# Kernel tuning notes

Measured on AMD Instinct MI355X. Metric: run time of the kernel, lower is better.

The kernel has to match this reference:

```python
import jax, jax.numpy as jnp
import numpy as np

DIM = 512; HEADS = 8; DH = 64; M = 256; ITERS = 6; N_PATCH = 10000; N_CLASSES = 2


def layernorm(x, w, b, eps=1e-5):
    mu = x.mean(-1, keepdims=True)
    var = ((x - mu) ** 2).mean(-1, keepdims=True)
    return (x - mu) * jax.lax.rsqrt(var + eps) * w + b


def pinv_iter(x, iters=ITERS):
    # Moore-Penrose iterative pseudo-inverse (lucidrains nystrom-attention)
    abs_x = jnp.abs(x)
    col = abs_x.sum(-1)
    row = abs_x.sum(-2)
    z = jnp.swapaxes(x, -1, -2) / (jnp.max(col) * jnp.max(row))
    I = jnp.eye(x.shape[-1], dtype=x.dtype)
    for _ in range(iters):
        xz = x @ z
        z = 0.25 * z @ (13 * I - xz @ (15 * I - xz @ (7 * I - xz)))
    return z


def nystrom_attn(x, qkv_w, out_w, out_b, res_w):
    b, n, _ = x.shape
    pad = (-n) % M  # front-pad so n divisible by num_landmarks
    xp = jnp.pad(x, ((0, 0), (pad, 0), (0, 0)))
    npad = n + pad
    qkv = (xp @ qkv_w).reshape(b, npad, 3, HEADS, DH)
    q = jnp.transpose(qkv[:, :, 0], (0, 2, 1, 3)) * (DH ** -0.5)  # [b,h,n,d]
    k = jnp.transpose(qkv[:, :, 1], (0, 2, 1, 3))
    v = jnp.transpose(qkv[:, :, 2], (0, 2, 1, 3))
    l = npad // M
    q_l = q.reshape(b, HEADS, M, l, DH).mean(3)  # landmark means [b,h,m,d]
    k_l = k.reshape(b, HEADS, M, l, DH).mean(3)
    attn1 = jax.nn.softmax(jnp.einsum('bhnd,bhmd->bhnm', q, k_l), -1)
    attn2 = jax.nn.softmax(jnp.einsum('bhid,bhjd->bhij', q_l, k_l), -1)
    attn3 = jax.nn.softmax(jnp.einsum('bhmd,bhnd->bhmn', q_l, k), -1)
    out = (attn1 @ pinv_iter(attn2)) @ (attn3 @ v)  # [b,h,n,d]
    pk = (res_w.shape[2] - 1) // 2
    out = out + jax.lax.conv_general_dilated(
        v, res_w, (1, 1), [(pk, pk), (0, 0)], feature_group_count=HEADS)
    out = jnp.transpose(out, (0, 2, 1, 3)).reshape(b, npad, HEADS * DH)
    out = out @ out_w + out_b
    return out[:, -n:]


def ppeg(x, H, W, w7, b7, w5, b5, w3, b3):
    B, _, C = x.shape
    cls_tok, feat = x[:, :1], x[:, 1:]
    f = jnp.transpose(feat, (0, 2, 1)).reshape(B, C, H, W)
    def dw(w, b):
        p = w.shape[2] // 2
        return jax.lax.conv_general_dilated(
            f, w, (1, 1), [(p, p), (p, p)], feature_group_count=C) + b[None, :, None, None]
    y = f + dw(w7, b7) + dw(w5, b5) + dw(w3, b3)
    y = jnp.transpose(y.reshape(B, C, H * W), (0, 2, 1))
    return jnp.concatenate([cls_tok, y], axis=1)


def setup_inputs() -> dict:
    key = jax.random.key(0)
    ks = jax.random.split(key, 16)
    d = {
        'x': jax.random.normal(ks[0], (1, N_PATCH, DIM), jnp.float32),
        'cls_token': jax.random.normal(ks[1], (1, 1, DIM), jnp.float32) * 1e-6,
        'ln1_w': jnp.ones((DIM,), jnp.float32), 'ln1_b': jnp.zeros((DIM,), jnp.float32),
        'qkv1_w': jax.random.normal(ks[2], (DIM, 3 * DIM), jnp.float32) * 0.03,
        'out1_w': jax.random.normal(ks[3], (DIM, DIM), jnp.float32) * 0.04,
        'out1_b': jnp.zeros((DIM,), jnp.float32),
        'res1_w': jax.random.normal(ks[4], (HEADS, 1, 33, 1), jnp.float32) * 0.1,
        'p7_w': jax.random.normal(ks[5], (DIM, 1, 7, 7), jnp.float32) * 0.1,
        'p7_b': jnp.zeros((DIM,), jnp.float32),
        'p5_w': jax.random.normal(ks[6], (DIM, 1, 5, 5), jnp.float32) * 0.1,
        'p5_b': jnp.zeros((DIM,), jnp.float32),
        'p3_w': jax.random.normal(ks[7], (DIM, 1, 3, 3), jnp.float32) * 0.1,
        'p3_b': jnp.zeros((DIM,), jnp.float32),
        'ln2_w': jnp.ones((DIM,), jnp.float32), 'ln2_b': jnp.zeros((DIM,), jnp.float32),
        'qkv2_w': jax.random.normal(ks[8], (DIM, 3 * DIM), jnp.float32) * 0.03,
        'out2_w': jax.random.normal(ks[9], (DIM, DIM), jnp.float32) * 0.04,
        'out2_b': jnp.zeros((DIM,), jnp.float32),
        'res2_w': jax.random.normal(ks[10], (HEADS, 1, 33, 1), jnp.float32) * 0.1,
        'norm_w': jnp.ones((DIM,), jnp.float32), 'norm_b': jnp.zeros((DIM,), jnp.float32),
        'fc2_w': jax.random.normal(ks[11], (DIM, N_CLASSES), jnp.float32) * 0.06,
        'fc2_b': jnp.zeros((N_CLASSES,), jnp.float32),
        'pc_w': jax.random.normal(ks[12], (DIM, N_CLASSES), jnp.float32) * 0.06,
        'pc_b': jnp.zeros((N_CLASSES,), jnp.float32),
    }
    return d


def reference(x, cls_token, ln1_w, ln1_b, qkv1_w, out1_w, out1_b, res1_w,
              p7_w, p7_b, p5_w, p5_b, p3_w, p3_b,
              ln2_w, ln2_b, qkv2_w, out2_w, out2_b, res2_w,
              norm_w, norm_b, fc2_w, fc2_b, pc_w, pc_b):
    h = x.astype(jnp.float32)
    B, n0, C = h.shape
    _H = int(np.ceil(np.sqrt(n0))); _W = _H
    add = _H * _W - n0
    if add > 0:
        h = jnp.concatenate([h, h[:, :add]], axis=1)
    h = jnp.concatenate([jnp.broadcast_to(cls_token, (B, 1, C)), h], axis=1)
    h = h + nystrom_attn(layernorm(h, ln1_w, ln1_b), qkv1_w, out1_w, out1_b, res1_w)
    h = ppeg(h, _H, _W, p7_w, p7_b, p5_w, p5_b, p3_w, p3_b)
    h = h + nystrom_attn(layernorm(h, ln2_w, ln2_b), qkv2_w, out2_w, out2_b, res2_w)
    hn = layernorm(h, norm_w, norm_b)
    cls_f = hn[:, 0]
    patch_f = hn[:, 1:]
    if add > 0:
        patch_f = patch_f[:, :n0]
    bag_logits = cls_f @ fc2_w + fc2_b
    patch_logits = patch_f @ pc_w + pc_b
    patch_scores = jax.nn.softmax(patch_logits, -1)
    return bag_logits, patch_logits, patch_scores
```

## Files before the change

### kernel.cpp

```cpp
#include <hip/hip_runtime.h>
#include <hip/hip_bf16.h>

#define DIM    512
#define HEADS  8
#define DHD    64
#define MLAND  256
#define NTOK   10001
#define NPATCH 10000
#define NPAD   10240
#define PADR   239
#define LFAC   40
#define MOUT   10112
#define NSPLIT 8

typedef __bf16 bf16x8_t __attribute__((ext_vector_type(8)));
typedef float  f32x4_t  __attribute__((ext_vector_type(4)));
typedef short  short8_t __attribute__((ext_vector_type(8)));

__device__ inline bf16x8_t bzero8() {
    union { short8_t s; bf16x8_t b; } u;
    u.s = (short8_t){0, 0, 0, 0, 0, 0, 0, 0};
    return u.b;
}

#define GLDS(gp, lp) __builtin_amdgcn_global_load_lds( \
    (const __attribute__((address_space(1))) void*)(gp), \
    (__attribute__((address_space(3))) void*)(lp), 16, 0, 0)

__global__ void k_concat(const float* __restrict__ x, const float* __restrict__ cls,
                         float* __restrict__ h) {
    int idx = blockIdx.x * 256 + threadIdx.x;
    if (idx >= NTOK * DIM) return;
    int row = idx / DIM, col = idx % DIM;
    h[idx] = (row == 0) ? cls[col] : x[(row - 1) * DIM + col];
}

__global__ void k_layernorm_bf(const float* __restrict__ h, const float* __restrict__ w,
                               const float* __restrict__ b, __hip_bfloat16* __restrict__ xbf) {
    int row = blockIdx.x;
    const float* r = h + (long)row * DIM;
    int t = threadIdx.x;
    float v0 = r[t], v1 = r[t + 256];
    __shared__ float red[256];
    red[t] = v0 + v1; __syncthreads();
    for (int o = 128; o > 0; o >>= 1) { if (t < o) red[t] += red[t + o]; __syncthreads(); }
    float mu = red[0] * (1.f / DIM); __syncthreads();
    float d0 = v0 - mu, d1 = v1 - mu;
    red[t] = d0 * d0 + d1 * d1; __syncthreads();
    for (int o = 128; o > 0; o >>= 1) { if (t < o) red[t] += red[t + o]; __syncthreads(); }
    float rstd = rsqrtf(red[0] * (1.f / DIM) + 1e-5f);
    long base = (long)(PADR + row) * DIM;
    xbf[base + t]       = __float2bfloat16(d0 * rstd * w[t] + b[t]);
    xbf[base + t + 256] = __float2bfloat16(d1 * rstd * w[t + 256] + b[t + 256]);
}

__global__ void k_zerobf(__hip_bfloat16* __restrict__ p, int n) {
    int i = blockIdx.x * 256 + threadIdx.x;
    if (i < n) p[i] = __float2bfloat16(0.f);
}
__global__ void k_wt_cvt(const float* __restrict__ W, __hip_bfloat16* __restrict__ Wt,
                         int K, int N) {
    __shared__ float tile[32][33];
    int k0 = blockIdx.x * 32, n0 = blockIdx.y * 32;
    int lx = threadIdx.x % 32, ly = threadIdx.x / 32;
    for (int i = 0; i < 32; i += 8) tile[ly + i][lx] = W[(long)(k0 + ly + i) * N + n0 + lx];
    __syncthreads();
    for (int i = 0; i < 32; i += 8)
        Wt[(long)(n0 + ly + i) * K + k0 + lx] = __float2bfloat16(tile[lx][ly + i]);
}
__global__ void k_vt(const __hip_bfloat16* __restrict__ vh, __hip_bfloat16* __restrict__ vt) {
    __shared__ __hip_bfloat16 tile[32][33];
    int n0 = blockIdx.x * 32, d0 = blockIdx.y * 32, h = blockIdx.z;
    int lx = threadIdx.x % 32, ly = threadIdx.x / 32;
    for (int i = 0; i < 32; i += 8)
        tile[ly + i][lx] = vh[((long)h * NPAD + n0 + ly + i) * 64 + d0 + lx];
    __syncthreads();
    for (int i = 0; i < 32; i += 8)
        vt[((long)h * 64 + d0 + ly + i) * NPAD + n0 + lx] = tile[lx][ly + i];
}

__global__ __launch_bounds__(256) void k_qkv_gemm(
    const __hip_bfloat16* __restrict__ A, const __hip_bfloat16* __restrict__ Bt,
    __hip_bfloat16* __restrict__ qh, __hip_bfloat16* __restrict__ kh,
    __hip_bfloat16* __restrict__ vh)
{
    const int K = 512;
    __shared__ unsigned short As[128 * 64];
    __shared__ unsigned short Bs[128 * 64];
    int tid = threadIdx.x;
    int m0 = blockIdx.y * 128, n0 = blockIdx.x * 128;
    int wave = tid >> 6, lane = tid & 63;
    int wm = (wave & 1) * 64, wn = (wave >> 1) * 64;
    f32x4_t zero4 = {0.f, 0.f, 0.f, 0.f};
    f32x4_t acc[4][4];
#pragma unroll
    for (int i = 0; i < 4; i++)
#pragma unroll
        for (int j = 0; j < 4; j++) acc[i][j] = zero4;
    int quad = lane >> 4, fr = lane & 15;
    int lrow8 = lane >> 3, gls = lane & 7;
    int gg = gls ^ lrow8;

    for (int k0 = 0; k0 < K; k0 += 64) {
        __syncthreads();
#pragma unroll
        for (int rnd = 0; rnd < 4; rnd++) {
            int r0 = rnd * 32 + wave * 8;
            int ar = r0 + lrow8;
            GLDS(A  + (long)(m0 + ar) * K + k0 + gg * 8, &As[r0 * 64]);
            GLDS(Bt + (long)(n0 + ar) * K + k0 + gg * 8, &Bs[r0 * 64]);
        }
        __syncthreads();
#pragma unroll
        for (int ks = 0; ks < 2; ks++) {
            int sg = (ks * 4 + quad) ^ (fr & 7);
            bf16x8_t af[4], bq[4];
#pragma unroll
            for (int i = 0; i < 4; i++) {
                af[i] = *(const bf16x8_t*)&As[(wm + i * 16 + fr) * 64 + sg * 8];
                bq[i] = *(const bf16x8_t*)&Bs[(wn + i * 16 + fr) * 64 + sg * 8];
            }
#pragma unroll
            for (int i = 0; i < 4; i++)
#pragma unroll
                for (int j = 0; j < 4; j++)
                    acc[i][j] = __builtin_amdgcn_mfma_f32_16x16x32_bf16(af[i], bq[j], acc[i][j], 0, 0, 0);
        }
    }
    int col = lane & 15, rq = lane >> 4;
#pragma unroll
    for (int j = 0; j < 4; j++) {
        int c = n0 + wn + j * 16 + col;
        int sect = c >> 9;
        int hh = (c >> 6) & 7;
        int d = c & 63;
        __hip_bfloat16* dst = (sect == 0) ? qh : (sect == 1) ? kh : vh;
        float sc = (sect == 0) ? 0.125f : 1.f;
#pragma unroll
        for (int i = 0; i < 4; i++) {
            int rbase = m0 + wm + i * 16 + rq * 4;
#pragma unroll
            for (int rr = 0; rr < 4; rr++) {
                int r = rbase + rr;
                dst[((long)hh * NPAD + r) * 64 + d] = __float2bfloat16(acc[i][j][rr] * sc);
            }
        }
    }
}

__global__ __launch_bounds__(256) void k_mfma_gemm(
    const __hip_bfloat16* __restrict__ A, const __hip_bfloat16* __restrict__ Bt,
    float* __restrict__ C, int M, int N, int K, int Mstore,
    const float* __restrict__ bias, int accum)
{
    __shared__ unsigned short As[128 * 64];
    __shared__ unsigned short Bs[128 * 64];
    int tid = threadIdx.x;
    int m0 = blockIdx.y * 128, n0 = blockIdx.x * 128;
    int wave = tid >> 6, lane = tid & 63;
    int wm = (wave & 1) * 64, wn = (wave >> 1) * 64;
    f32x4_t zero4 = {0.f, 0.f, 0.f, 0.f};
    f32x4_t acc[4][4];
#pragma unroll
    for (int i = 0; i < 4; i++)
#pragma unroll
        for (int j = 0; j < 4; j++) acc[i][j] = zero4;
    int quad = lane >> 4, fr = lane & 15;
    int lrow8 = lane >> 3, gls = lane & 7;
    int gg = gls ^ lrow8;

    for (int k0 = 0; k0 < K; k0 += 64) {
        __syncthreads();
#pragma unroll
        for (int rnd = 0; rnd < 4; rnd++) {
            int r0 = rnd * 32 + wave * 8;
            int ar = r0 + lrow8;
            GLDS(A  + (long)(m0 + ar) * K + k0 + gg * 8, &As[r0 * 64]);
            GLDS(Bt + (long)(n0 + ar) * K + k0 + gg * 8, &Bs[r0 * 64]);
        }
        __syncthreads();
#pragma unroll
        for (int ks = 0; ks < 2; ks++) {
            int sg = (ks * 4 + quad) ^ (fr & 7);
            bf16x8_t af[4], bq[4];
#pragma unroll
            for (int i = 0; i < 4; i++) {
                af[i] = *(const bf16x8_t*)&As[(wm + i * 16 + fr) * 64 + sg * 8];
                bq[i] = *(const bf16x8_t*)&Bs[(wn + i * 16 + fr) * 64 + sg * 8];
            }
#pragma unroll
            for (int i = 0; i < 4; i++)
#pragma unroll
                for (int j = 0; j < 4; j++)
                    acc[i][j] = __builtin_amdgcn_mfma_f32_16x16x32_bf16(af[i], bq[j], acc[i][j], 0, 0, 0);
        }
    }
    int col = lane & 15, rq = lane >> 4;
#pragma unroll
    for (int j = 0; j < 4; j++) {
        int c = n0 + wn + j * 16 + col;
        float bsv = bias ? bias[c] : 0.f;
#pragma unroll
        for (int i = 0; i < 4; i++) {
            int rbase = m0 + wm + i * 16 + rq * 4;
#pragma unroll
            for (int rr = 0; rr < 4; rr++) {
                int r = rbase + rr;
                if (r >= Mstore) continue;
                float v = acc[i][j][rr] + bsv;
                long off = (long)r * N + c;
                if (accum) C[off] += v; else C[off] = v;
            }
        }
    }
}

__global__ __launch_bounds__(256) void k_mfma_t64(
    const __hip_bfloat16* __restrict__ A, long lda, long abatch, int arowmax,
    const __hip_bfloat16* __restrict__ Bt, long ldb, long bbatch,
    __hip_bfloat16* __restrict__ Cbf, long ldc, long cbatch, int ksplit)
{
    int h = blockIdx.z;
    const __hip_bfloat16* Ab = A + (long)h * abatch;
    const __hip_bfloat16* Bb = Bt + (long)h * bbatch;
    int m0 = blockIdx.y * 128;
    int kbeg = blockIdx.x * ksplit, kend = kbeg + ksplit;
    int wave = threadIdx.x >> 6, lane = threadIdx.x & 63;
    int wm = (wave & 1) * 64, wn = (wave >> 1) * 32;
    int fr = lane & 15, quad = lane >> 4;
    f32x4_t zero4 = {0.f, 0.f, 0.f, 0.f};
    f32x4_t acc[4][2];
#pragma unroll
    for (int i = 0; i < 4; i++) { acc[i][0] = zero4; acc[i][1] = zero4; }
    for (int k0 = kbeg; k0 < kend; k0 += 32) {
        bf16x8_t bq[2];
#pragma unroll
        for (int j = 0; j < 2; j++)
            bq[j] = *(const bf16x8_t*)(Bb + (long)(wn + j * 16 + fr) * ldb + k0 + quad * 8);
#pragma unroll
        for (int i = 0; i < 4; i++) {
            int r = m0 + wm + i * 16 + fr;
            bf16x8_t af = (r < arowmax) ? *(const bf16x8_t*)(Ab + (long)r * lda + k0 + quad * 8)
                                        : bzero8();
#pragma unroll
            for (int j = 0; j < 2; j++)
                acc[i][j] = __builtin_amdgcn_mfma_f32_16x16x32_bf16(af, bq[j], acc[i][j], 0, 0, 0);
        }
    }
#pragma unroll
    for (int i = 0; i < 4; i++)
#pragma unroll
        for (int j = 0; j < 2; j++)
#pragma unroll
            for (int rr = 0; rr < 4; rr++) {
                int r = m0 + wm + i * 16 + quad * 4 + rr;
                int c = wn + j * 16 + fr;
                Cbf[(long)h * cbatch + (long)c * ldc + r] = __float2bfloat16(acc[i][j][rr]);
            }
}

__global__ __launch_bounds__(256) void k_mm256(
    const __hip_bfloat16* __restrict__ Aa, const __hip_bfloat16* __restrict__ Bt,
    float s, float acoef, const __hip_bfloat16* __restrict__ Aadd,
    __hip_bfloat16* __restrict__ Ca, __hip_bfloat16* __restrict__ Ct)
{
    int hd = blockIdx.z;
    long hb = (long)hd * 65536;
    int m0 = blockIdx.y * 64, n0 = blockIdx.x * 32;
    int wave = threadIdx.x >> 6, lane = threadIdx.x & 63;
    int fr = lane & 15, quad = lane >> 4;
    int mrow = m0 + wave * 16;
    f32x4_t zero4 = {0.f, 0.f, 0.f, 0.f};
    f32x4_t acc[2];
    acc[0] = zero4; acc[1] = zero4;
#pragma unroll
    for (int k0 = 0; k0 < 256; k0 += 32) {
        bf16x8_t af = *(const bf16x8_t*)(Aa + hb + (long)(mrow + fr) * 256 + k0 + quad * 8);
#pragma unroll
        for (int j = 0; j < 2; j++) {
            bf16x8_t bq = *(const bf16x8_t*)(Bt + hb + (long)(n0 + j * 16 + fr) * 256 + k0 + quad * 8);
            acc[j] = __builtin_amdgcn_mfma_f32_16x16x32_bf16(af, bq, acc[j], 0, 0, 0);
        }
    }
#pragma unroll
    for (int j = 0; j < 2; j++)
#pragma unroll
        for (int rr = 0; rr < 4; rr++) {
            int r = mrow + quad * 4 + rr;
            int c = n0 + j * 16 + fr;
            float v = s * acc[j][rr];
            if (Aadd) v += acoef * __bfloat162float(Aadd[hb + (long)r * 256 + c]);
            __hip_bfloat16 bv = __float2bfloat16(v);
            if (Ca) Ca[hb + (long)r * 256 + c] = bv;
            if (Ct) Ct[hb + (long)c * 256 + r] = bv;
        }
}

__global__ __launch_bounds__(256) void k_attn3f(
    const __hip_bfloat16* __restrict__ qlbf, const __hip_bfloat16* __restrict__ kh,
    const __hip_bfloat16* __restrict__ vt, float* __restrict__ part)
{
    int ns = blockIdx.x, mt = blockIdx.y, h = blockIdx.z;
    int wave = threadIdx.x >> 6, lane = threadIdx.x & 63;
    int fr = lane & 15, quad = lane >> 4;
    int lrow8 = lane >> 3, gls = lane & 7;
    int gg = gls ^ lrow8;
    int vsub = lane >> 5, vgrp = lane & 31;
    int swz = fr & 7;
    __shared__ unsigned short Ks[2][256 * 64];
    __shared__ unsigned short Vs[2][64 * 256];
    __shared__ __hip_bfloat16 Pl[64 * 136];
    f32x4_t zero4 = {0.f, 0.f, 0.f, 0.f};
    bf16x8_t aq[2];
    {
        const __hip_bfloat16* qb = qlbf + (long)h * 16384 + (long)(mt * 64 + wave * 16 + fr) * 64;
        aq[0] = *(const bf16x8_t*)(qb + quad * 8);
        aq[1] = *(const bf16x8_t*)(qb + 32 + quad * 8);
    }
    f32x4_t O[4];
#pragma unroll
    for (int j = 0; j < 4; j++) O[j] = zero4;
    float mr[4] = {-1e30f, -1e30f, -1e30f, -1e30f};
    float lr[4] = {0.f, 0.f, 0.f, 0.f};
    const __hip_bfloat16* kb = kh + (long)h * NPAD * 64;
    const __hip_bfloat16* vb = vt + (long)h * 64 * NPAD;

#define STAGE_KV(N0, KD, VD) do { \
    _Pragma("unroll") \
    for (int rnd = 0; rnd < 8; rnd++) { \
        int r0 = rnd * 32 + wave * 8; \
        GLDS(kb + (long)((N0) + r0 + lrow8) * 64 + gg * 8, (KD) + r0 * 64); \
    } \
    _Pragma("unroll") \
    for (int rnd = 0; rnd < 8; rnd++) { \
        int v0 = rnd * 8 + wave * 2; \
        int vrow = v0 + vsub; \
        GLDS(vb + (long)vrow * NPAD + (N0) + (vgrp ^ (vrow & 7)) * 8, (VD) + v0 * 256); \
    } \
} while (0)

    STAGE_KV(ns * 1280, &Ks[0][0], &Vs[0][0]);

    for (int nt = 0; nt < 5; nt++) {
        int bsel = nt & 1;
        if (nt < 4) {
            int n1 = ns * 1280 + (nt + 1) * 256;
            STAGE_KV(n1, &Ks[bsel ^ 1][0], &Vs[bsel ^ 1][0]);
            asm volatile("s_waitcnt vmcnt(16)" ::: "memory");
        } else {
            asm volatile("s_waitcnt vmcnt(0)" ::: "memory");
        }
        __builtin_amdgcn_s_barrier();

        const unsigned short* Kc = &Ks[bsel][0];
        const unsigned short* Vc = &Vs[bsel][0];
        f32x4_t s[16];
#pragma unroll
        for (int j = 0; j < 16; j++) s[j] = zero4;
#pragma unroll
        for (int j = 0; j < 16; j++) {
            const unsigned short* kr = Kc + (j * 16 + fr) * 64;
            bf16x8_t b0 = *(const bf16x8_t*)(kr + (quad ^ swz) * 8);
            bf16x8_t b1 = *(const bf16x8_t*)(kr + ((quad ^ swz) ^ 4) * 8);
            s[j] = __builtin_amdgcn_mfma_f32_16x16x32_bf16(aq[0], b0, s[j], 0, 0, 0);
            s[j] = __builtin_amdgcn_mfma_f32_16x16x32_bf16(aq[1], b1, s[j], 0, 0, 0);
        }
        float tm[4] = {-1e30f, -1e30f, -1e30f, -1e30f};
#pragma unroll
        for (int j = 0; j < 16; j++)
#pragma unroll
            for (int rr = 0; rr < 4; rr++) tm[rr] = fmaxf(tm[rr], s[j][rr]);
#pragma unroll
        for (int rr = 0; rr < 4; rr++) {
#pragma unroll
            for (int o = 8; o > 0; o >>= 1) tm[rr] = fmaxf(tm[rr], __shfl_xor(tm[rr], o));
        }
        float alpha[4], ts[4];
#pragma unroll
        for (int rr = 0; rr < 4; rr++) {
            float mnew = fmaxf(mr[rr], tm[rr]);
            alpha[rr] = __expf(mr[rr] - mnew);
            mr[rr] = mnew;
            ts[rr] = 0.f;
        }
#pragma unroll
        for (int j = 0; j < 16; j++)
#pragma unroll
            for (int rr = 0; rr < 4; rr++) {
                float e = __expf(s[j][rr] - mr[rr]);
                s[j][rr] = e;
                ts[rr] += e;
            }
#pragma unroll
        for (int rr = 0; rr < 4; rr++) {
#pragma unroll
            for (int o = 8; o > 0; o >>= 1) ts[rr] += __shfl_xor(ts[rr], o);
            lr[rr] = lr[rr] * alpha[rr] + ts[rr];
        }
#pragma unroll
        for (int j = 0; j < 4; j++)
#pragma unroll
            for (int rr = 0; rr < 4; rr++) O[j][rr] *= alpha[rr];
#pragma unroll
        for (int half = 0; half < 2; half++) {
#pragma unroll
            for (int j = 0; j < 8; j++)
#pragma unroll
                for (int rr = 0; rr < 4; rr++)
                    Pl[(wave * 16 + quad * 4 + rr) * 136 + j * 16 + fr] =
                        __float2bfloat16(s[half * 8 + j][rr]);
#pragma unroll
            for (int k0 = 0; k0 < 128; k0 += 32) {
                bf16x8_t af = *(const bf16x8_t*)&Pl[(wave * 16 + fr) * 136 + k0 + quad * 8];
                int gb = (half * 128 + k0) >> 3;
#pragma unroll
                for (int j = 0; j < 4; j++) {
                    const unsigned short* vr = Vc + (j * 16 + fr) * 256;
                    bf16x8_t bq = *(const bf16x8_t*)(vr + ((gb + quad) ^ swz) * 8);
                    O[j] = __builtin_amdgcn_mfma_f32_16x16x32_bf16(af, bq, O[j], 0, 0, 0);
                }
            }
        }
        asm volatile("" ::: "memory");
        __builtin_amdgcn_s_barrier();
    }
#undef STAGE_KV

    float* Ob = part + (long)((h * 4 + mt) * NSPLIT + ns) * 4224;
#pragma unroll
    for (int j = 0; j < 4; j++)
#pragma unroll
        for (int rr = 0; rr < 4; rr++)
            Ob[(wave * 16 + quad * 4 + rr) * 64 + j * 16 + fr] = O[j][rr];
    if (fr == 0) {
#pragma unroll
        for (int rr = 0; rr < 4; rr++) {
            Ob[4096 + wave * 16 + quad * 4 + rr] = mr[rr];
            Ob[4160 + wave * 16 + quad * 4 + rr] = lr[rr];
        }
    }
}

__global__ void k_a3comb(const float* __restrict__ part, __hip_bfloat16* __restrict__ a3vt) {
    int mt = blockIdx.x, h = blockIdx.y, t = threadIdx.x;
    int row = t >> 2, c0 = (t & 3) * 16;
    long base = (long)((h * 4 + mt) * NSPLIT) * 4224;
    float M = -1e30f;
    for (int s = 0; s < NSPLIT; s++) M = fmaxf(M, part[base + s * 4224 + 4096 + row]);
    float L = 0.f;
    float o[16];
#pragma unroll
    for (int c = 0; c < 16; c++) o[c] = 0.f;
    for (int s = 0; s < NSPLIT; s++) {
        const float* pb = part + base + (long)s * 4224;
        float w = __expf(pb[4096 + row] - M);
        L += pb[4160 + row] * w;
#pragma unroll
        for (int c = 0; c < 16; c++) o[c] += w * pb[row * 64 + c0 + c];
    }
    float invL = 1.f / L;
#pragma unroll
    for (int c = 0; c < 16; c++)
        a3vt[(long)h * 16384 + (long)(c0 + c) * 256 + mt * 64 + row] = __float2bfloat16(o[c] * invL);
}

__global__ void k_conv_res(const __hip_bfloat16* __restrict__ vh, const float* __restrict__ resw,
                           __hip_bfloat16* __restrict__ convbf) {
    int e4 = blockIdx.x * 256 + threadIdx.x;
    if (e4 >= NTOK * 128) return;
    int i = e4 >> 7;
    int c4 = (e4 & 127) * 4;
    int hh = c4 >> 6, d = c4 & 63;
    int n = PADR + i;
    const __hip_bfloat16* vb = vh + (long)hh * NPAD * 64 + d;
    float a0 = 0.f, a1 = 0.f, a2 = 0.f, a3 = 0.f;
#pragma unroll
    for (int t = 0; t < 33; t++) {
        int nn = n - 16 + t;
        if (nn < NPAD) {
            float w = resw[hh * 33 + t];
            uint2 pv = *(const uint2*)(vb + (long)nn * 64);
            __hip_bfloat16 vv[4];
            *(uint2*)vv = pv;
            a0 += w * __bfloat162float(vv[0]);
            a1 += w * __bfloat162float(vv[1]);
            a2 += w * __bfloat162float(vv[2]);
            a3 += w * __bfloat162float(vv[3]);
        }
    }
    __hip_bfloat16 o[4] = {__float2bfloat16(a0), __float2bfloat16(a1),
                           __float2bfloat16(a2), __float2bfloat16(a3)};
    *(uint2*)(convbf + (long)i * DIM + c4) = *(uint2*)o;
}

__global__ __launch_bounds__(256, 4) void k_attn1f(
    const __hip_bfloat16* __restrict__ qh, const __hip_bfloat16* __restrict__ klbf,
    const __hip_bfloat16* __restrict__ w2bt, const __hip_bfloat16* __restrict__ convbf,
    __hip_bfloat16* __restrict__ abf)
{
    int h = blockIdx.y;
    int i0 = blockIdx.x * 32;
    __shared__ __hip_bfloat16 Pl[64 * 136];
    __shared__ float mS[2][2][16][2];
    int tid = threadIdx.x;
    int wave = tid >> 6, lane = tid & 63;
    int rg = wave & 1, lh = wave >> 1;
    int fr = lane & 15, quad = lane >> 4;
    const __hip_bfloat16* kb = klbf + (long)h * (MLAND * DHD) + (long)lh * 128 * DHD;
    f32x4_t zero4 = {0.f, 0.f, 0.f, 0.f};

    f32x4_t s[8];
#pragma unroll
    for (int j = 0; j < 8; j++) s[j] = zero4;
    int arow = i0 + rg * 16 + fr;
    const __hip_bfloat16* qrow = qh + ((long)h * NPAD + PADR + arow) * 64;
#pragma unroll
    for (int k0 = 0; k0 < 64; k0 += 32) {
        bf16x8_t af = (arow < NTOK) ? *(const bf16x8_t*)(qrow + k0 + quad * 8) : bzero8();
#pragma unroll
        for (int j = 0; j < 8; j++) {
            bf16x8_t bq = *(const bf16x8_t*)(kb + (long)(j * 16 + fr) * DHD + k0 + quad * 8);
            s[j] = __builtin_amdgcn_mfma_f32_16x16x32_bf16(af, bq, s[j], 0, 0, 0);
        }
    }
    float mx[4] = {-1e30f, -1e30f, -1e30f, -1e30f};
#pragma unroll
    for (int j = 0; j < 8; j++)
#pragma unroll
        for (int rr = 0; rr < 4; rr++) mx[rr] = fmaxf(mx[rr], s[j][rr]);
#pragma unroll
    for (int rr = 0; rr < 4; rr++) {
#pragma unroll
        for (int o = 8; o > 0; o >>= 1) mx[rr] = fmaxf(mx[rr], __shfl_xor(mx[rr], o));
    }
    float sum[4] = {0.f, 0.f, 0.f, 0.f};
#pragma unroll
    for (int j = 0; j < 8; j++)
#pragma unroll
        for (int rr = 0; rr < 4; rr++) {
            float e = __expf(s[j][rr] - mx[rr]);
            s[j][rr] = e;
            sum[rr] += e;
        }
#pragma unroll
    for (int rr = 0; rr < 4; rr++) {
#pragma unroll
        for (int o = 8; o > 0; o >>= 1) sum[rr] += __shfl_xor(sum[rr], o);
    }
    if (fr == 0) {
#pragma unroll
        for (int rr = 0; rr < 4; rr++) {
            mS[lh][rg][quad * 4 + rr][0] = mx[rr];
            mS[lh][rg][quad * 4 + rr][1] = sum[rr];
        }
    }
#pragma unroll
    for (int j = 0; j < 8; j++)
#pragma unroll
        for (int rr = 0; rr < 4; rr++)
            Pl[(wave * 16 + quad * 4 + rr) * 136 + j * 16 + fr] = __float2bfloat16(s[j][rr]);
    __syncthreads();
    float fac[4];
#pragma unroll
    for (int rr = 0; rr < 4; rr++) {
        int r16 = quad * 4 + rr;
        float pm = mS[lh ^ 1][rg][r16][0], pS = mS[lh ^ 1][rg][r16][1];
        float M = fmaxf(mx[rr], pm);
        float sw = __expf(mx[rr] - M);
        float tot = sum[rr] * sw + pS * __expf(pm - M);
        fac[rr] = sw / tot;
    }
    const __hip_bfloat16* wb = w2bt + (long)h * (DHD * MLAND) + lh * 128;
    f32x4_t oc[4];
#pragma unroll
    for (int j = 0; j < 4; j++) oc[j] = zero4;
#pragma unroll
    for (int k0 = 0; k0 < 128; k0 += 32) {
        bf16x8_t af = *(const bf16x8_t*)&Pl[(wave * 16 + fr) * 136 + k0 + quad * 8];
#pragma unroll
        for (int j = 0; j < 4; j++) {
            bf16x8_t bq = *(const bf16x8_t*)(wb + (long)(j * 16 + fr) * MLAND + k0 + quad * 8);
            oc[j] = __builtin_amdgcn_mfma_f32_16x16x32_bf16(af, bq, oc[j], 0, 0, 0);
        }
    }
#pragma unroll
    for (int j = 0; j < 4; j++)
#pragma unroll
        for (int rr = 0; rr < 4; rr++) oc[j][rr] *= fac[rr];
    __syncthreads();
    float* ex = (float*)Pl;
    if (lh == 1) {
#pragma unroll
        for (int j = 0; j < 4; j++)
#pragma unroll
            for (int rr = 0; rr < 4; rr++)
                ex[(rg * 16 + quad * 4 + rr) * 64 + j * 16 + fr] = oc[j][rr];
    }
    __syncthreads();
    if (lh == 0) {
        float cp[4][4];
#pragma unroll
        for (int j = 0; j < 4; j++)
#pragma unroll
            for (int rr = 0; rr < 4; rr++) {
                int r = i0 + rg * 16 + quad * 4 + rr;
                cp[j][rr] = (r < NTOK)
                    ? __bfloat162float(convbf[(long)r * DIM + h * DHD + j * 16 + fr]) : 0.f;
            }
#pragma unroll
        for (int j = 0; j < 4; j++)
#pragma unroll
            for (int rr = 0; rr < 4; rr++) {
                int r = i0 + rg * 16 + quad * 4 + rr;
                if (r < NTOK) {
                    float v = oc[j][rr] + ex[(rg * 16 + quad * 4 + rr) * 64 + j * 16 + fr]
                              + cp[j][rr];
                    abf[(long)r * DIM + h * DHD + j * 16 + fr] = __float2bfloat16(v);
                }
            }
    }
}

__global__ void k_landmarks(const __hip_bfloat16* __restrict__ qh,
                            const __hip_bfloat16* __restrict__ kh,
                            float* __restrict__ ql, float* __restrict__ kl,
                            __hip_bfloat16* __restrict__ qlbf, __hip_bfloat16* __restrict__ klbf) {
    int m = blockIdx.x, h = blockIdx.y, d = threadIdx.x;
    float sq = 0.f, sk = 0.f;
    for (int j = 0; j < LFAC; j++) {
        long base = ((long)h * NPAD + m * LFAC + j) * 64 + d;
        sq += __bfloat162float(qh[base]);
        sk += __bfloat162float(kh[base]);
    }
    long o = ((long)h * MLAND + m) * DHD + d;
    float vq = sq * (1.f / LFAC), vk = sk * (1.f / LFAC);
    ql[o] = vq; kl[o] = vk;
    qlbf[o] = __float2bfloat16(vq);
    klbf[o] = __float2bfloat16(vk);
}

__global__ void k_attn2(const float* __restrict__ ql, const float* __restrict__ kl,
                        float* __restrict__ attn2, __hip_bfloat16* __restrict__ attn2bf) {
    int i = blockIdx.x, h = blockIdx.y, j = threadIdx.x;
    __shared__ float q[64];
    __shared__ float red[256];
    if (j < 64) q[j] = ql[((long)h * MLAND + i) * DHD + j];
    __syncthreads();
    const float* kr = kl + ((long)h * MLAND + j) * DHD;
    float s = 0.f;
#pragma unroll 8
    for (int d = 0; d < 64; d++) s += q[d] * kr[d];
    red[j] = s; __syncthreads();
    for (int o = 128; o > 0; o >>= 1) { if (j < o) red[j] = fmaxf(red[j], red[j + o]); __syncthreads(); }
    float mx = red[0]; __syncthreads();
    float e = __expf(s - mx);
    red[j] = e; __syncthreads();
    for (int o = 128; o > 0; o >>= 1) { if (j < o) red[j] += red[j + o]; __syncthreads(); }
    float v = e / red[0];
    long off = ((long)h * MLAND + i) * MLAND + j;
    attn2[off] = v;
    attn2bf[off] = __float2bfloat16(v);
}

__global__ void k_colrow(const float* __restrict__ x, float* __restrict__ scal) {
    int h = blockIdx.x, t = threadIdx.x;
    const float* xh = x + (long)h * MLAND * MLAND;
    float cs = 0.f, rs = 0.f;
    for (int j = 0; j < MLAND; j++) {
        cs += fabsf(xh[(long)t * MLAND + j]);
        rs += fabsf(xh[(long)j * MLAND + t]);
    }
    __shared__ float red[256];
    red[t] = cs; __syncthreads();
    for (int o = 128; o > 0; o >>= 1) { if (t < o) red[t] = fmaxf(red[t], red[t + o]); __syncthreads(); }
    if (t == 0) scal[2 + h] = red[0];
    __syncthreads();
    red[t] = rs; __syncthreads();
    for (int o = 128; o > 0; o >>= 1) { if (t < o) red[t] = fmaxf(red[t], red[t + o]); __syncthreads(); }
    if (t == 0) scal[10 + h] = red[0];
}

__global__ void k_tscale2(const float* __restrict__ x, const float* __restrict__ scal,
                          __hip_bfloat16* __restrict__ za, __hip_bfloat16* __restrict__ zt) {
    int h = blockIdx.z;
    int tj = blockIdx.x * 32, ti = blockIdx.y * 32;
    __shared__ float tile[32][33];
    const float* xh = x + (long)h * 65536;
    int lx = threadIdx.x % 32, ly = threadIdx.x / 32;
    float cm = scal[2], rm = scal[10];
#pragma unroll
    for (int k = 1; k < 8; k++) {
        cm = fmaxf(cm, scal[2 + k]);
        rm = fmaxf(rm, scal[10 + k]);
    }
    float inv = 1.f / (cm * rm);
    for (int yy = 0; yy < 32; yy += 8) {
        float v = xh[(long)(ti + ly + yy) * MLAND + tj + lx];
        tile[ly + yy][lx] = v;
        zt[(long)h * 65536 + (long)(ti + ly + yy) * MLAND + tj + lx] = __float2bfloat16(v * inv);
    }
    __syncthreads();
    for (int yy = 0; yy < 32; yy += 8)
        za[(long)h * 65536 + (long)(tj + ly + yy) * MLAND + ti + lx] =
            __float2bfloat16(tile[lx][ly + yy] * inv);
}

__global__ void k_tfwd(const float* __restrict__ h, float* __restrict__ ft) {
    __shared__ float tile[32][33];
    int t0 = blockIdx.x * 32, c0 = blockIdx.y * 32;
    int lx = threadIdx.x % 32, ly = threadIdx.x / 32;
    for (int i = 0; i < 32; i += 8) {
        int t = t0 + ly + i;
        if (t < NPATCH) tile[ly + i][lx] = h[(long)(1 + t) * DIM + c0 + lx];
    }
    __syncthreads();
    for (int i = 0; i < 32; i += 8) {
        int c = c0 + ly + i, t = t0 + lx;
        if (t < NPATCH) ft[(long)c * NPATCH + t] = tile[lx][ly + i];
    }
}

__global__ __launch_bounds__(256) void k_ppeg2(
    const float* __restrict__ ft, float* __restrict__ yt,
    const float* __restrict__ w7, const float* __restrict__ b7,
    const float* __restrict__ w5, const float* __restrict__ b5,
    const float* __restrict__ w3, const float* __restrict__ b3)
{
    int s = blockIdx.x, c = blockIdx.y;
    __shared__ float tile[26][106];
    __shared__ float wt[49];
    int tid = threadIdx.x;
    int r0 = s * 20 - 3;
    for (int idx = tid; idx < 26 * 106; idx += 256) {
        int rr = idx / 106, cc = idx % 106;
        int gy = r0 + rr, gx = cc - 3;
        float v = 0.f;
        if (gy >= 0 && gy < 100 && gx >= 0 && gx < 100)
            v = ft[(long)c * NPATCH + gy * 100 + gx];
        tile[rr][cc] = v;
    }
    if (tid < 49) {
        int dy = tid / 7 - 3, dx = tid % 7 - 3;
        float w = w7[c * 49 + tid];
        if (dy >= -2 && dy <= 2 && dx >= -2 && dx <= 2) w += w5[c * 25 + (dy + 2) * 5 + (dx + 2)];
        if (dy >= -1 && dy <= 1 && dx >= -1 && dx <= 1) w += w3[c * 9 + (dy + 1) * 3 + (dx + 1)];
        wt[tid] = w;
    }
    __syncthreads();
    float bsum = b7[c] + b5[c] + b3[c];
    for (int p = tid; p < 2000; p += 256) {
        int ly = p / 100, lx = p % 100;
        float acc = tile[ly + 3][lx + 3] + bsum;
#pragma unroll
        for (int dy = 0; dy < 7; dy++)
#pragma unroll
            for (int dx = 0; dx < 7; dx++)
                acc += wt[dy * 7 + dx] * tile[ly + dy][lx + dx];
        yt[(long)c * NPATCH + (s * 20 + ly) * 100 + lx] = acc;
    }
}

__global__ void k_tback(const float* __restrict__ yt, float* __restrict__ h) {
    __shared__ float tile[32][33];
    int t0 = blockIdx.x * 32, c0 = blockIdx.y * 32;
    int lx = threadIdx.x % 32, ly = threadIdx.x / 32;
    for (int i = 0; i < 32; i += 8) {
        int c = c0 + ly + i, t = t0 + lx;
        if (t < NPATCH) tile[ly + i][lx] = yt[(long)c * NPATCH + t];
    }
    __syncthreads();
    for (int i = 0; i < 32; i += 8) {
        int t = t0 + ly + i;
        if (t < NPATCH) h[(long)(1 + t) * DIM + c0 + lx] = tile[lx][ly + i];
    }
}

__global__ void k_final(const float* __restrict__ h, const float* __restrict__ nw,
                        const float* __restrict__ nb,
                        const float* __restrict__ fc2w, const float* __restrict__ fc2b,
                        const float* __restrict__ pcw, const float* __restrict__ pcb,
                        float* __restrict__ out)
{
    int row = blockIdx.x;
    int t = threadIdx.x;
    const float* r = h + (long)row * DIM;
    float v0 = r[t], v1 = r[t + 256];
    __shared__ float red[256];
    red[t] = v0 + v1; __syncthreads();
    for (int o = 128; o > 0; o >>= 1) { if (t < o) red[t] += red[t + o]; __syncthreads(); }
    float mu = red[0] * (1.f / DIM); __syncthreads();
    float d0 = v0 - mu, d1 = v1 - mu;
    red[t] = d0 * d0 + d1 * d1; __syncthreads();
    for (int o = 128; o > 0; o >>= 1) { if (t < o) red[t] += red[t + o]; __syncthreads(); }
    float rstd = rsqrtf(red[0] * (1.f / DIM) + 1e-5f); __syncthreads();
    float h0 = d0 * rstd * nw[t] + nb[t];
    float h1 = d1 * rstd * nw[t + 256] + nb[t + 256];
    const float* w = (row == 0) ? fc2w : pcw;
    float p0 = h0 * w[t * 2] + h1 * w[(t + 256) * 2];
    float p1 = h0 * w[t * 2 + 1] + h1 * w[(t + 256) * 2 + 1];
    red[t] = p0; __syncthreads();
    for (int o = 128; o > 0; o >>= 1) { if (t < o) red[t] += red[t + o]; __syncthreads(); }
    float l0 = red[0]; __syncthreads();
    red[t] = p1; __syncthreads();
    for (int o = 128; o > 0; o >>= 1) { if (t < o) red[t] += red[t + o]; __syncthreads(); }
    if (t == 0) {
        float l1 = red[0];
        const float* bb = (row == 0) ? fc2b : pcb;
        float a0 = l0 + bb[0], a1 = l1 + bb[1];
        if (row == 0) { out[0] = a0; out[1] = a1; }
        else {
            long i = row - 1;
            out[2 + i * 2] = a0;
            out[2 + i * 2 + 1] = a1;
            float m = fmaxf(a0, a1);
            float e0 = __expf(a0 - m), e1 = __expf(a1 - m);
            float inv = 1.f / (e0 + e1);
            out[2 + 2 * NPATCH + i * 2] = e0 * inv;
            out[2 + 2 * NPATCH + i * 2 + 1] = e1 * inv;
        }
    }
}

extern "C" void kernel_launch(void* const* d_in, const int* in_sizes, int n_in,
                              void* d_out, int out_size, void* d_ws, size_t ws_size,
                              hipStream_t stream)
{
    const float* x     = (const float*)d_in[0];
    const float* cls   = (const float*)d_in[1];
    const float* ln1w  = (const float*)d_in[2];
    const float* ln1b  = (const float*)d_in[3];
    const float* qkv1w = (const float*)d_in[4];
    const float* out1w = (const float*)d_in[5];
    const float* out1b = (const float*)d_in[6];
    const float* res1w = (const float*)d_in[7];
    const float* p7w   = (const float*)d_in[8];
    const float* p7b   = (const float*)d_in[9];
    const float* p5w   = (const float*)d_in[10];
    const float* p5b   = (const float*)d_in[11];
    const float* p3w   = (const float*)d_in[12];
    const float* p3b   = (const float*)d_in[13];
    const float* ln2w  = (const float*)d_in[14];
    const float* ln2b  = (const float*)d_in[15];
    const float* qkv2w = (const float*)d_in[16];
    const float* out2w = (const float*)d_in[17];
    const float* out2b = (const float*)d_in[18];
    const float* res2w = (const float*)d_in[19];
    const float* normw = (const float*)d_in[20];
    const float* normb = (const float*)d_in[21];
    const float* fc2w  = (const float*)d_in[22];
    const float* fc2b  = (const float*)d_in[23];
    const float* pcw   = (const float*)d_in[24];
    const float* pcb   = (const float*)d_in[25];
    float* out = (float*)d_out;

    float* p = (float*)d_ws;
    float* h      = p; p += 5120512;
    float* yt     = p; p += 5120512;
    float* ql     = p; p += 131072;
    float* kl     = p; p += 131072;
    float* x2     = p; p += 524288;
    float* scal   = p; p += 32;
    float* part   = p; p += 1081344;
    float* ft     = p; p += 5120512;
    __hip_bfloat16* qh     = (__hip_bfloat16*)p; p += 2621440;
    __hip_bfloat16* kh     = (__hip_bfloat16*)p; p += 2621440;
    __hip_bfloat16* vh     = (__hip_bfloat16*)p; p += 2621440;
    __hip_bfloat16* xbf    = (__hip_bfloat16*)p; p += 2621440;
    __hip_bfloat16* abf    = (__hip_bfloat16*)p; p += 2588672;
    __hip_bfloat16* convbf = (__hip_bfloat16*)p; p += 2560256;
    __hip_bfloat16* qw1t   = (__hip_bfloat16*)p; p += 393216;
    __hip_bfloat16* qw2t   = (__hip_bfloat16*)p; p += 393216;
    __hip_bfloat16* ow1t   = (__hip_bfloat16*)p; p += 131072;
    __hip_bfloat16* ow2t   = (__hip_bfloat16*)p; p += 131072;
    __hip_bfloat16* x2a    = (__hip_bfloat16*)p; p += 262144;
    __hip_bfloat16* za     = (__hip_bfloat16*)p; p += 262144;
    __hip_bfloat16* zt     = (__hip_bfloat16*)p; p += 262144;
    __hip_bfloat16* za2    = (__hip_bfloat16*)p; p += 262144;
    __hip_bfloat16* zt2    = (__hip_bfloat16*)p; p += 262144;
    __hip_bfloat16* xza    = (__hip_bfloat16*)p; p += 262144;
    __hip_bfloat16* xzt    = (__hip_bfloat16*)p; p += 262144;
    __hip_bfloat16* t1t    = (__hip_bfloat16*)p; p += 262144;
    __hip_bfloat16* t2t    = (__hip_bfloat16*)p; p += 262144;
    __hip_bfloat16* qlbf   = (__hip_bfloat16*)p; p += 65536;
    __hip_bfloat16* klbf   = (__hip_bfloat16*)p; p += 65536;
    __hip_bfloat16* vt     = (__hip_bfloat16*)p; p += 2621440;
    __hip_bfloat16* a3vt   = (__hip_bfloat16*)p; p += 65536;
    __hip_bfloat16* w2bt   = (__hip_bfloat16*)p; p += 65536;

    k_concat<<<dim3((NTOK * DIM + 255) / 256), 256, 0, stream>>>(x, cls, h);
    k_wt_cvt<<<dim3(16, 48), 256, 0, stream>>>(qkv1w, qw1t, 512, 1536);
    k_wt_cvt<<<dim3(16, 48), 256, 0, stream>>>(qkv2w, qw2t, 512, 1536);
    k_wt_cvt<<<dim3(16, 16), 256, 0, stream>>>(out1w, ow1t, 512, 512);
    k_wt_cvt<<<dim3(16, 16), 256, 0, stream>>>(out2w, ow2t, 512, 512);
    k_zerobf<<<dim3((PADR * DIM + 255) / 256), 256, 0, stream>>>(xbf, PADR * DIM);

    auto layer = [&](const float* lnw, const float* lnb, const __hip_bfloat16* qwt,
                     const __hip_bfloat16* owt, const float* outb, const float* resw) {
        k_layernorm_bf<<<NTOK, 256, 0, stream>>>(h, lnw, lnb, xbf);
        k_qkv_gemm<<<dim3(12, 80), 256, 0, stream>>>(xbf, qwt, qh, kh, vh);
        k_vt<<<dim3(320, 2, HEADS), 256, 0, stream>>>(vh, vt);
        k_landmarks<<<dim3(MLAND, HEADS), 64, 0, stream>>>(qh, kh, ql, kl, qlbf, klbf);
        k_attn2<<<dim3(MLAND, HEADS), 256, 0, stream>>>(ql, kl, x2, x2a);
        k_colrow<<<HEADS, 256, 0, stream>>>(x2, scal);
        k_tscale2<<<dim3(8, 8, HEADS), 256, 0, stream>>>(x2, scal, za, zt);
        {
            __hip_bfloat16 *zra = za, *zrt = zt, *zoa = za2, *zot = zt2;
            dim3 g(8, 4, HEADS);
            for (int it = 0; it < 6; it++) {
                k_mm256<<<g, 256, 0, stream>>>(x2a, zrt, 1.f, 0.f, nullptr, xza, xzt);
                k_mm256<<<g, 256, 0, stream>>>(xza, xzt, -1.f, 7.f, xza, nullptr, t1t);
                k_mm256<<<g, 256, 0, stream>>>(xza, t1t, -1.f, 15.f, xza, nullptr, t2t);
                k_mm256<<<g, 256, 0, stream>>>(zra, t2t, -0.25f, 3.25f, zra, zoa, zot);
                __hip_bfloat16* tmp;
                tmp = zra; zra = zoa; zoa = tmp;
                tmp = zrt; zrt = zot; zot = tmp;
            }
        }
        k_attn3f<<<dim3(NSPLIT, 4, HEADS), 256, 0, stream>>>(qlbf, kh, vt, part);
        k_a3comb<<<dim3(4, HEADS), 256, 0, stream>>>(part, a3vt);
        k_mfma_t64<<<dim3(1, 2, HEADS), 256, 0, stream>>>(
            za, 256, 65536, 256, a3vt, 256, 16384,
            w2bt, 256, 16384, 256);
        k_conv_res<<<dim3((NTOK * 128 + 255) / 256), 256, 0, stream>>>(vh, resw, convbf);
        k_attn1f<<<dim3(313, HEADS), 256, 0, stream>>>(qh, klbf, w2bt, convbf, abf);
        k_mfma_gemm<<<dim3(4, 79), 256, 0, stream>>>(abf, owt, h, MOUT, 512, 512,
                                                     NTOK, outb, 1);
    };

    layer(ln1w, ln1b, qw1t, ow1t, out1b, res1w);

    k_tfwd<<<dim3(313, 16), 256, 0, stream>>>(h, ft);
    k_ppeg2<<<dim3(5, 512), 256, 0, stream>>>(ft, yt, p7w, p7b, p5w, p5b, p3w, p3b);
    k_tback<<<dim3(313, 16), 256, 0, stream>>>(yt, h);

    layer(ln2w, ln2b, qw2t, ow2t, out2b, res2w);

    k_final<<<NTOK, 256, 0, stream>>>(h, normw, normb, fc2w, fc2b, pcw, pcb, out);
    (void)in_sizes; (void)n_in; (void)out_size; (void)ws_size;
}
```

Baseline: 974.6 us.

## Fuse pseudo-inverse iterations into one persistent kernel with grid barriers

Replaces the 24 per-layer small GEMM launches of the Moore-Penrose iteration with a single persistent kernel. Its 256 blocks synchronise between phases through an atomic counter barrier, and the counter is reset inside k_tscale2. This removes launch and drain overhead between tiny dependent GEMMs, but it depends on every block being co-resident, since otherwise the barrier can deadlock. Separately, attn1f drops the max subtraction in its softmax and hoists the residual conv loads to the start of the kernel. Dropping the max saves shuffles and exps but risks fp32 overflow if logits ever get large.

```diff
diff --git a/kernel.cpp b/kernel.cpp
--- a/kernel.cpp
+++ b/kernel.cpp
@@ -259,17 +259,12 @@
             }
 }
 
-__global__ __launch_bounds__(256) void k_mm256(
-    const __hip_bfloat16* __restrict__ Aa, const __hip_bfloat16* __restrict__ Bt,
-    float s, float acoef, const __hip_bfloat16* __restrict__ Aadd,
-    __hip_bfloat16* __restrict__ Ca, __hip_bfloat16* __restrict__ Ct)
+__device__ __forceinline__ void mm_phase(
+    const __hip_bfloat16* Aa, const __hip_bfloat16* Bt,
+    float s, float acoef, const __hip_bfloat16* Aadd,
+    __hip_bfloat16* Ca, __hip_bfloat16* Ct,
+    long hb, int mrow, int n0, int fr, int quad)
 {
-    int hd = blockIdx.z;
-    long hb = (long)hd * 65536;
-    int m0 = blockIdx.y * 64, n0 = blockIdx.x * 32;
-    int wave = threadIdx.x >> 6, lane = threadIdx.x & 63;
-    int fr = lane & 15, quad = lane >> 4;
-    int mrow = m0 + wave * 16;
     f32x4_t zero4 = {0.f, 0.f, 0.f, 0.f};
     f32x4_t acc[2];
     acc[0] = zero4; acc[1] = zero4;
@@ -294,6 +289,49 @@
             if (Ca) Ca[hb + (long)r * 256 + c] = bv;
             if (Ct) Ct[hb + (long)c * 256 + r] = bv;
         }
+}
+
+__device__ __forceinline__ void pinv_sync(int* cnt, int target) {
+    __syncthreads();
+    __threadfence();
+    if (threadIdx.x == 0) {
+        __hip_atomic_fetch_add(cnt, 1, __ATOMIC_RELAXED, __HIP_MEMORY_SCOPE_AGENT);
+        while (__hip_atomic_load(cnt, __ATOMIC_RELAXED, __HIP_MEMORY_SCOPE_AGENT) < target)
+            __builtin_amdgcn_s_sleep(2);
+    }
+    __syncthreads();
+    __threadfence();
+}
+
+__global__ __launch_bounds__(256) void k_pinv(
+    const __hip_bfloat16* __restrict__ x2a,
+    __hip_bfloat16* __restrict__ za,  __hip_bfloat16* __restrict__ zt,
+    __hip_bfloat16* __restrict__ za2, __hip_bfloat16* __restrict__ zt2,
+    __hip_bfloat16* __restrict__ xza, __hip_bfloat16* __restrict__ xzt,
+    __hip_bfloat16* __restrict__ t1t, __hip_bfloat16* __restrict__ t2t,
+    int* cnt)
+{
+    int hd = blockIdx.z;
+    long hb = (long)hd * 65536;
+    int m0 = blockIdx.y * 64, n0 = blockIdx.x * 32;
+    int wave = threadIdx.x >> 6, lane = threadIdx.x & 63;
+    int fr = lane & 15, quad = lane >> 4;
+    int mrow = m0 + wave * 16;
+    __hip_bfloat16 *zra = za, *zrt = zt, *zoa = za2, *zot = zt2;
+    int ph = 0;
+    for (int it = 0; it < 6; it++) {
+        mm_phase(x2a, zrt, 1.f, 0.f, nullptr, xza, xzt, hb, mrow, n0, fr, quad);
+        pinv_sync(cnt, ++ph * 256);
+        mm_phase(xza, xzt, -1.f, 7.f, xza, nullptr, t1t, hb, mrow, n0, fr, quad);
+        pinv_sync(cnt, ++ph * 256);
+        mm_phase(xza, t1t, -1.f, 15.f, xza, nullptr, t2t, hb, mrow, n0, fr, quad);
+        pinv_sync(cnt, ++ph * 256);
+        mm_phase(zra, t2t, -0.25f, 3.25f, zra, zoa, zot, hb, mrow, n0, fr, quad);
+        if (it < 5) pinv_sync(cnt, ++ph * 256);
+        __hip_bfloat16* tmp;
+        tmp = zra; zra = zoa; zoa = tmp;
+        tmp = zrt; zrt = zot; zot = tmp;
+    }
 }
 
 __global__ __launch_bounds__(256) void k_attn3f(
@@ -501,7 +539,7 @@
     int h = blockIdx.y;
     int i0 = blockIdx.x * 32;
     __shared__ __hip_bfloat16 Pl[64 * 136];
-    __shared__ float mS[2][2][16][2];
+    __shared__ float mS[2][2][16];
     int tid = threadIdx.x;
     int wave = tid >> 6, lane = tid & 63;
     int rg = wave & 1, lh = wave >> 1;
@@ -509,96 +547,8 @@
     const __hip_bfloat16* kb = klbf + (long)h * (MLAND * DHD) + (long)lh * 128 * DHD;
     f32x4_t zero4 = {0.f, 0.f, 0.f, 0.f};
 
-    f32x4_t s[8];
-#pragma unroll
-    for (int j = 0; j < 8; j++) s[j] = zero4;
-    int arow = i0 + rg * 16 + fr;
-    const __hip_bfloat16* qrow = qh + ((long)h * NPAD + PADR + arow) * 64;
-#pragma unroll
-    for (int k0 = 0; k0 < 64; k0 += 32) {
-        bf16x8_t af = (arow < NTOK) ? *(const bf16x8_t*)(qrow + k0 + quad * 8) : bzero8();
-#pragma unroll
-        for (int j = 0; j < 8; j++) {
-            bf16x8_t bq = *(const bf16x8_t*)(kb + (long)(j * 16 + fr) * DHD + k0 + quad * 8);
-            s[j] = __builtin_amdgcn_mfma_f32_16x16x32_bf16(af, bq, s[j], 0, 0, 0);
-        }
-    }
-    float mx[4] = {-1e30f, -1e30f, -1e30f, -1e30f};
-#pragma unroll
-    for (int j = 0; j < 8; j++)
-#pragma unroll
-        for (int rr = 0; rr < 4; rr++) mx[rr] = fmaxf(mx[rr], s[j][rr]);
-#pragma unroll
-    for (int rr = 0; rr < 4; rr++) {
-#pragma unroll
-        for (int o = 8; o > 0; o >>= 1) mx[rr] = fmaxf(mx[rr], __shfl_xor(mx[rr], o));
-    }
-    float sum[4] = {0.f, 0.f, 0.f, 0.f};
-#pragma unroll
-    for (int j = 0; j < 8; j++)
-#pragma unroll
-        for (int rr = 0; rr < 4; rr++) {
-            float e = __expf(s[j][rr] - mx[rr]);
-            s[j][rr] = e;
-            sum[rr] += e;
-        }
-#pragma unroll
-    for (int rr = 0; rr < 4; rr++) {
-#pragma unroll
-        for (int o = 8; o > 0; o >>= 1) sum[rr] += __shfl_xor(sum[rr], o);
-    }
-    if (fr == 0) {
-#pragma unroll
-        for (int rr = 0; rr < 4; rr++) {
-            mS[lh][rg][quad * 4 + rr][0] = mx[rr];
-            mS[lh][rg][quad * 4 + rr][1] = sum[rr];
-        }
-    }
-#pragma unroll
-    for (int j = 0; j < 8; j++)
-#pragma unroll
-        for (int rr = 0; rr < 4; rr++)
-            Pl[(wave * 16 + quad * 4 + rr) * 136 + j * 16 + fr] = __float2bfloat16(s[j][rr]);
-    __syncthreads();
-    float fac[4];
-#pragma unroll
-    for (int rr = 0; rr < 4; rr++) {
-        int r16 = quad * 4 + rr;
-        float pm = mS[lh ^ 1][rg][r16][0], pS = mS[lh ^ 1][rg][r16][1];
-        float M = fmaxf(mx[rr], pm);
-        float sw = __expf(mx[rr] - M);
-        float tot = sum[rr] * sw + pS * __expf(pm - M);
-        fac[rr] = sw / tot;
-    }
-    const __hip_bfloat16* wb = w2bt + (long)h * (DHD * MLAND) + lh * 128;
-    f32x4_t oc[4];
-#pragma unroll
-    for (int j = 0; j < 4; j++) oc[j] = zero4;
-#pragma unroll
-    for (int k0 = 0; k0 < 128; k0 += 32) {
-        bf16x8_t af = *(const bf16x8_t*)&Pl[(wave * 16 + fr) * 136 + k0 + quad * 8];
-#pragma unroll
-        for (int j = 0; j < 4; j++) {
-            bf16x8_t bq = *(const bf16x8_t*)(wb + (long)(j * 16 + fr) * MLAND + k0 + quad * 8);
-            oc[j] = __builtin_amdgcn_mfma_f32_16x16x32_bf16(af, bq, oc[j], 0, 0, 0);
-        }
-    }
-#pragma unroll
-    for (int j = 0; j < 4; j++)
-#pragma unroll
-        for (int rr = 0; rr < 4; rr++) oc[j][rr] *= fac[rr];
-    __syncthreads();
-    float* ex = (float*)Pl;
-    if (lh == 1) {
-#pragma unroll
-        for (int j = 0; j < 4; j++)
-#pragma unroll
-            for (int rr = 0; rr < 4; rr++)
-                ex[(rg * 16 + quad * 4 + rr) * 64 + j * 16 + fr] = oc[j][rr];
-    }
-    __syncthreads();
+    float cp[4][4];
     if (lh == 0) {
-        float cp[4][4];
 #pragma unroll
         for (int j = 0; j < 4; j++)
 #pragma unroll
@@ -607,6 +557,78 @@
                 cp[j][rr] = (r < NTOK)
                     ? __bfloat162float(convbf[(long)r * DIM + h * DHD + j * 16 + fr]) : 0.f;
             }
+    }
+
+    f32x4_t s[8];
+#pragma unroll
+    for (int j = 0; j < 8; j++) s[j] = zero4;
+    int arow = i0 + rg * 16 + fr;
+    const __hip_bfloat16* qrow = qh + ((long)h * NPAD + PADR + arow) * 64;
+#pragma unroll
+    for (int k0 = 0; k0 < 64; k0 += 32) {
+        bf16x8_t af = (arow < NTOK) ? *(const bf16x8_t*)(qrow + k0 + quad * 8) : bzero8();
+#pragma unroll
+        for (int j = 0; j < 8; j++) {
+            bf16x8_t bq = *(const bf16x8_t*)(kb + (long)(j * 16 + fr) * DHD + k0 + quad * 8);
+            s[j] = __builtin_amdgcn_mfma_f32_16x16x32_bf16(af, bq, s[j], 0, 0, 0);
+        }
+    }
+    float sum[4] = {0.f, 0.f, 0.f, 0.f};
+#pragma unroll
+    for (int j = 0; j < 8; j++)
+#pragma unroll
+        for (int rr = 0; rr < 4; rr++) {
+            float e = __expf(s[j][rr]);
+            s[j][rr] = e;
+            sum[rr] += e;
+        }
+#pragma unroll
+    for (int rr = 0; rr < 4; rr++) {
+#pragma unroll
+        for (int o = 8; o > 0; o >>= 1) sum[rr] += __shfl_xor(sum[rr], o);
+    }
+    if (fr == 0) {
+#pragma unroll
+        for (int rr = 0; rr < 4; rr++) mS[lh][rg][quad * 4 + rr] = sum[rr];
+    }
+#pragma unroll
+    for (int j = 0; j < 8; j++)
+#pragma unroll
+        for (int rr = 0; rr < 4; rr++)
+            Pl[(wave * 16 + quad * 4 + rr) * 136 + j * 16 + fr] = __float2bfloat16(s[j][rr]);
+    __syncthreads();
+    float fac[4];
+#pragma unroll
+    for (int rr = 0; rr < 4; rr++)
+        fac[rr] = 1.f / (sum[rr] + mS[lh ^ 1][rg][quad * 4 + rr]);
+    const __hip_bfloat16* wb = w2bt + (long)h * (DHD * MLAND) + lh * 128;
+    f32x4_t oc[4];
+#pragma unroll
+    for (int j = 0; j < 4; j++) oc[j] = zero4;
+#pragma unroll
+    for (int k0 = 0; k0 < 128; k0 += 32) {
+        bf16x8_t af = *(const bf16x8_t*)&Pl[(wave * 16 + fr) * 136 + k0 + quad * 8];
+#pragma unroll
+        for (int j = 0; j < 4; j++) {
+            bf16x8_t bq = *(const bf16x8_t*)(wb + (long)(j * 16 + fr) * MLAND + k0 + quad * 8);
+            oc[j] = __builtin_amdgcn_mfma_f32_16x16x32_bf16(af, bq, oc[j], 0, 0, 0);
+        }
+    }
+#pragma unroll
+    for (int j = 0; j < 4; j++)
+#pragma unroll
+        for (int rr = 0; rr < 4; rr++) oc[j][rr] *= fac[rr];
+    __syncthreads();
+    float* ex = (float*)Pl;
+    if (lh == 1) {
+#pragma unroll
+        for (int j = 0; j < 4; j++)
+#pragma unroll
+            for (int rr = 0; rr < 4; rr++)
+                ex[(rg * 16 + quad * 4 + rr) * 64 + j * 16 + fr] = oc[j][rr];
+    }
+    __syncthreads();
+    if (lh == 0) {
 #pragma unroll
         for (int j = 0; j < 4; j++)
 #pragma unroll
@@ -681,10 +703,13 @@
 }
 
 __global__ void k_tscale2(const float* __restrict__ x, const float* __restrict__ scal,
-                          __hip_bfloat16* __restrict__ za, __hip_bfloat16* __restrict__ zt) {
+                          __hip_bfloat16* __restrict__ za, __hip_bfloat16* __restrict__ zt,
+                          int* __restrict__ cnt) {
     int h = blockIdx.z;
     int tj = blockIdx.x * 32, ti = blockIdx.y * 32;
     __shared__ float tile[32][33];
+    if (threadIdx.x == 0 && blockIdx.x == 0 && blockIdx.y == 0 && blockIdx.z == 0)
+        cnt[0] = 0;
     const float* xh = x + (long)h * 65536;
     int lx = threadIdx.x % 32, ly = threadIdx.x / 32;
     float cm = scal[2], rm = scal[10];
@@ -860,6 +885,7 @@
     float* kl     = p; p += 131072;
     float* x2     = p; p += 524288;
     float* scal   = p; p += 32;
+    int*   pinvc  = (int*)p; p += 32;
     float* part   = p; p += 1081344;
     float* ft     = p; p += 5120512;
     __hip_bfloat16* qh     = (__hip_bfloat16*)p; p += 2621440;
@@ -902,20 +928,9 @@
         k_landmarks<<<dim3(MLAND, HEADS), 64, 0, stream>>>(qh, kh, ql, kl, qlbf, klbf);
         k_attn2<<<dim3(MLAND, HEADS), 256, 0, stream>>>(ql, kl, x2, x2a);
         k_colrow<<<HEADS, 256, 0, stream>>>(x2, scal);
-        k_tscale2<<<dim3(8, 8, HEADS), 256, 0, stream>>>(x2, scal, za, zt);
-        {
-            __hip_bfloat16 *zra = za, *zrt = zt, *zoa = za2, *zot = zt2;
-            dim3 g(8, 4, HEADS);
-            for (int it = 0; it < 6; it++) {
-                k_mm256<<<g, 256, 0, stream>>>(x2a, zrt, 1.f, 0.f, nullptr, xza, xzt);
-                k_mm256<<<g, 256, 0, stream>>>(xza, xzt, -1.f, 7.f, xza, nullptr, t1t);
-                k_mm256<<<g, 256, 0, stream>>>(xza, t1t, -1.f, 15.f, xza, nullptr, t2t);
-                k_mm256<<<g, 256, 0, stream>>>(zra, t2t, -0.25f, 3.25f, zra, zoa, zot);
-                __hip_bfloat16* tmp;
-                tmp = zra; zra = zoa; zoa = tmp;
-                tmp = zrt; zrt = zot; zot = tmp;
-            }
-        }
+        k_tscale2<<<dim3(8, 8, HEADS), 256, 0, stream>>>(x2, scal, za, zt, pinvc);
+        k_pinv<<<dim3(8, 4, HEADS), 256, 0, stream>>>(x2a, za, zt, za2, zt2,
+                                                      xza, xzt, t1t, t2t, pinvc);
         k_attn3f<<<dim3(NSPLIT, 4, HEADS), 256, 0, stream>>>(qlbf, kh, vt, part);
         k_a3comb<<<dim3(4, HEADS), 256, 0, stream>>>(part, a3vt);
         k_mfma_t64<<<dim3(1, 2, HEADS), 256, 0, stream>>>(
```

Result: slower. 3.166 ms (+224.9%).
